# Optimization experiments

Hardware: AMD Instinct MI355X
Metric: run time of the kernel (lower is better)

## Reference

```python
import jax, jax.numpy as jnp
import numpy as np

K = 1024   # number of NNLS components (theta_1 is K x K)
B = 8192   # batched frames / columns


def setup_inputs() -> dict:
    key = jax.random.key(0)
    k1, k2, k3, k4 = jax.random.split(key, 4)
    # theta_1 = I - AtA / ||AtA||_F  -> near-identity contraction; emulate with
    # identity minus a small random symmetric-ish perturbation.
    pert = jax.random.normal(k1, (K, K), dtype=jnp.float32) * (1.0 / K)
    th1 = jnp.eye(K, dtype=jnp.float32) - pert
    Y = jax.random.uniform(k2, (K, B), dtype=jnp.float32)
    X_old = jax.random.uniform(k3, (K, B), dtype=jnp.float32)
    weight = jax.random.normal(k4, (K, B), dtype=jnp.float32) * 0.1  # theta_2 = Atb/n_AtA
    k = 2  # PGD iteration counter
    return {"th1": th1, "Y": Y, "X_old": X_old, "k": k, "weight": weight}


def reference(th1, Y, X_old, k, weight):
    # One projected-gradient-descent step of NNLS with Nesterov momentum:
    #   new_X = relu(th1 @ Y + weight)
    #   Y_new = new_X + (k-1)/(k+2) * (new_X - X_old)
    kf = jnp.float32(k)
    new_X = jax.nn.relu(jnp.matmul(th1, Y) + weight)          # [K, B]
    momentum = (kf - 1.0) / (kf + 2.0)
    Y_new = new_X + momentum * (new_X - X_old)                # [K, B]
    return (Y_new, new_X, k + 1, weight)
```

## Files before the change

### kernel.cpp

```cpp
#include <hip/hip_runtime.h>
#include <cstdint>


#define KDIM 1024
#define NDIM 8192
#define KB_ELEMS (1024UL * 8192UL)
#define LDA 40

typedef short short8 __attribute__((ext_vector_type(8)));
typedef float f32x4 __attribute__((ext_vector_type(4)));

struct __attribute__((aligned(4))) f4u { float x, y, z, w; };

__device__ __forceinline__ uint32_t pk2(float a, float b) {
  uint32_t ua = __builtin_bit_cast(uint32_t, a) + 0x8000u;
  uint32_t ub = __builtin_bit_cast(uint32_t, b) + 0x8000u;
  return (ua >> 16) | (ub & 0xFFFF0000u);
}

__global__ __launch_bounds__(512, 4) void nnls_gemm(
    const float* __restrict__ th1, const float* __restrict__ Y,
    const float* __restrict__ xold, const int* __restrict__ kin,
    const float* __restrict__ weight, float* __restrict__ out)
{
  __shared__ __align__(16) char smem[32768];
  unsigned short* As = (unsigned short*)smem;
  unsigned short* Bs = (unsigned short*)(smem + 10240);

  const int tid  = threadIdx.x;
  const int lane = tid & 63;
  const int w    = tid >> 6;
  const int wm = w >> 1, wn = w & 1;
  const int quad = lane >> 4, nl = lane & 15;

  const int m0 = blockIdx.y * 128;
  const int n0 = blockIdx.x * 128;

  const int ar = tid >> 3;
  const int ac = tid & 7;
  const float* abase = th1 + (size_t)(m0 + ar) * KDIM + ac * 4;

  const int bn = tid & 127;
  const int bk = (tid >> 7) * 8;
  const float* ybase = Y + (size_t)bk * NDIM + n0 + bn;

  float4 ab[2];
  float  yb[8];
  ab[0] = *(const float4*)(abase);
  ab[1] = *(const float4*)(abase + (size_t)64 * KDIM);
#pragma unroll
  for (int r = 0; r < 8; ++r) yb[r] = ybase[(size_t)r * NDIM];

  f32x4 acc[2][4] = {};

  for (int kt = 0; kt < 32; ++kt) {
    {
      uint2 d0; d0.x = pk2(ab[0].x, ab[0].y); d0.y = pk2(ab[0].z, ab[0].w);
      *(uint2*)&As[ar * LDA + ac * 4] = d0;
      uint2 d1; d1.x = pk2(ab[1].x, ab[1].y); d1.y = pk2(ab[1].z, ab[1].w);
      *(uint2*)&As[(ar + 64) * LDA + ac * 4] = d1;
      uint4 e;
      e.x = pk2(yb[0], yb[1]); e.y = pk2(yb[2], yb[3]);
      e.z = pk2(yb[4], yb[5]); e.w = pk2(yb[6], yb[7]);
      *(uint4*)&Bs[bn * LDA + bk] = e;
    }
    __syncthreads();

    if (kt < 31) {
      const float* an = abase + (kt + 1) * 32;
      ab[0] = *(const float4*)(an);
      ab[1] = *(const float4*)(an + (size_t)64 * KDIM);
      const float* yn = ybase + (size_t)((kt + 1) * 32) * NDIM;
#pragma unroll
      for (int r = 0; r < 8; ++r) yb[r] = yn[(size_t)r * NDIM];
    }

    short8 af[2], bf[4];
#pragma unroll
    for (int i = 0; i < 2; ++i)
      af[i] = *(const short8*)&As[(wm * 32 + i * 16 + nl) * LDA + quad * 8];
#pragma unroll
    for (int j = 0; j < 4; ++j)
      bf[j] = *(const short8*)&Bs[(wn * 64 + j * 16 + nl) * LDA + quad * 8];
#pragma unroll
    for (int i = 0; i < 2; ++i)
#pragma unroll
      for (int j = 0; j < 4; ++j)
        acc[i][j] = __builtin_amdgcn_mfma_f32_16x16x32_bf16(af[i], bf[j], acc[i][j], 0, 0, 0);

    __syncthreads();
  }

  const float kf  = (float)kin[0];
  const float mom = (kf - 1.0f) / (kf + 2.0f);
  float* ep = (float*)smem + w * 1024;
  const int lr = lane >> 2;
  const int cb = (lane & 3) * 16;
  const int swzR = 16 * ((lr >> 2) & 1) + 4 * (lr & 3);

#pragma unroll
  for (int i = 0; i < 2; ++i) {
#pragma unroll
    for (int j = 0; j < 4; ++j)
#pragma unroll
      for (int r = 0; r < 4; ++r) {
        const int wrow = quad * 4 + r;
        const int colp = (j * 16 + nl) ^ (16 * (quad & 1) + 4 * r);
        ep[wrow * 64 + colp] = acc[i][j][r];
      }
    __syncthreads();

    const int mg = m0 + wm * 32 + i * 16 + lr;
#pragma unroll
    for (int t = 0; t < 4; ++t) {
      const int colp = (cb + 4 * t) ^ swzR;
      const float4 cv = *(const float4*)&ep[lr * 64 + colp];
      const int ng = n0 + wn * 64 + cb + 4 * t;
      const size_t idx = (size_t)mg * NDIM + ng;
      const float4 wv = *(const float4*)&weight[idx];
      const float4 xo = *(const float4*)&xold[idx];
      float4 nx, yn;
      nx.x = fmaxf(cv.x + wv.x, 0.0f); nx.y = fmaxf(cv.y + wv.y, 0.0f);
      nx.z = fmaxf(cv.z + wv.z, 0.0f); nx.w = fmaxf(cv.w + wv.w, 0.0f);
      yn.x = nx.x + mom * (nx.x - xo.x); yn.y = nx.y + mom * (nx.y - xo.y);
      yn.z = nx.z + mom * (nx.z - xo.z); yn.w = nx.w + mom * (nx.w - xo.w);
      *(float4*)&out[idx] = yn;
      *(float4*)&out[KB_ELEMS + idx] = nx;
      f4u s; s.x = wv.x; s.y = wv.y; s.z = wv.z; s.w = wv.w;
      *(f4u*)&out[2 * KB_ELEMS + 1 + idx] = s;
    }
    __syncthreads();
  }

  if (blockIdx.x == 0 && blockIdx.y == 0 && tid == 0)
    out[2 * KB_ELEMS] = (float)(kin[0] + 1);
}

extern "C" void kernel_launch(void* const* d_in, const int* in_sizes, int n_in,
                              void* d_out, int out_size, void* d_ws, size_t ws_size,
                              hipStream_t stream) {
  const float* th1  = (const float*)d_in[0];
  const float* Y    = (const float*)d_in[1];
  const float* xold = (const float*)d_in[2];
  const int*   kin  = (const int*)d_in[3];
  const float* wgt  = (const float*)d_in[4];
  float* out = (float*)d_out;

  dim3 grid(NDIM / 128, KDIM / 128);
  nnls_gemm<<<grid, 512, 0, stream>>>(th1, Y, xold, kin, wgt, out);
}
```

Baseline: 251.7 us.

## Double-buffer LDS tiles and restructure epilogue to drop per-stage barriers

```diff
diff --git a/kernel.cpp b/kernel.cpp
--- a/kernel.cpp
+++ b/kernel.cpp
@@ -23,9 +23,11 @@
     const float* __restrict__ xold, const int* __restrict__ kin,
     const float* __restrict__ weight, float* __restrict__ out)
 {
-  __shared__ __align__(16) char smem[32768];
-  unsigned short* As = (unsigned short*)smem;
-  unsigned short* Bs = (unsigned short*)(smem + 10240);
+  __shared__ __align__(16) char smem[40960];
+  unsigned short* As0 = (unsigned short*)smem;
+  unsigned short* Bs0 = (unsigned short*)(smem + 10240);
+  unsigned short* As1 = (unsigned short*)(smem + 20480);
+  unsigned short* Bs1 = (unsigned short*)(smem + 30720);
 
   const int tid  = threadIdx.x;
   const int lane = tid & 63;
@@ -53,16 +55,20 @@
 
   f32x4 acc[2][4] = {};
 
+#pragma unroll 2
   for (int kt = 0; kt < 32; ++kt) {
+    unsigned short* Asp = (kt & 1) ? As1 : As0;
+    unsigned short* Bsp = (kt & 1) ? Bs1 : Bs0;
+
     {
       uint2 d0; d0.x = pk2(ab[0].x, ab[0].y); d0.y = pk2(ab[0].z, ab[0].w);
-      *(uint2*)&As[ar * LDA + ac * 4] = d0;
+      *(uint2*)&Asp[ar * LDA + ac * 4] = d0;
       uint2 d1; d1.x = pk2(ab[1].x, ab[1].y); d1.y = pk2(ab[1].z, ab[1].w);
-      *(uint2*)&As[(ar + 64) * LDA + ac * 4] = d1;
+      *(uint2*)&Asp[(ar + 64) * LDA + ac * 4] = d1;
       uint4 e;
       e.x = pk2(yb[0], yb[1]); e.y = pk2(yb[2], yb[3]);
       e.z = pk2(yb[4], yb[5]); e.w = pk2(yb[6], yb[7]);
-      *(uint4*)&Bs[bn * LDA + bk] = e;
+      *(uint4*)&Bsp[bn * LDA + bk] = e;
     }
     __syncthreads();
 
@@ -78,45 +84,39 @@
     short8 af[2], bf[4];
 #pragma unroll
     for (int i = 0; i < 2; ++i)
-      af[i] = *(const short8*)&As[(wm * 32 + i * 16 + nl) * LDA + quad * 8];
+      af[i] = *(const short8*)&Asp[(wm * 32 + i * 16 + nl) * LDA + quad * 8];
 #pragma unroll
     for (int j = 0; j < 4; ++j)
-      bf[j] = *(const short8*)&Bs[(wn * 64 + j * 16 + nl) * LDA + quad * 8];
+      bf[j] = *(const short8*)&Bsp[(wn * 64 + j * 16 + nl) * LDA + quad * 8];
 #pragma unroll
     for (int i = 0; i < 2; ++i)
 #pragma unroll
       for (int j = 0; j < 4; ++j)
         acc[i][j] = __builtin_amdgcn_mfma_f32_16x16x32_bf16(af[i], bf[j], acc[i][j], 0, 0, 0);
-
-    __syncthreads();
   }
+  __syncthreads();
 
   const float kf  = (float)kin[0];
   const float mom = (kf - 1.0f) / (kf + 2.0f);
-  float* ep = (float*)smem + w * 1024;
-  const int lr = lane >> 2;
-  const int cb = (lane & 3) * 16;
-  const int swzR = 16 * ((lr >> 2) & 1) + 4 * (lr & 3);
+  float* ep = (float*)smem + w * 1088;
+  const int u  = lane >> 4;
+  const int mc = lane & 15;
 
 #pragma unroll
   for (int i = 0; i < 2; ++i) {
 #pragma unroll
     for (int j = 0; j < 4; ++j)
 #pragma unroll
-      for (int r = 0; r < 4; ++r) {
-        const int wrow = quad * 4 + r;
-        const int colp = (j * 16 + nl) ^ (16 * (quad & 1) + 4 * r);
-        ep[wrow * 64 + colp] = acc[i][j][r];
-      }
-    __syncthreads();
+      for (int r = 0; r < 4; ++r)
+        ep[(quad * 4 + r) * 68 + (j * 16 + nl)] = acc[i][j][r];
 
-    const int mg = m0 + wm * 32 + i * 16 + lr;
+    const int mgb = m0 + wm * 32 + i * 16;
 #pragma unroll
     for (int t = 0; t < 4; ++t) {
-      const int colp = (cb + 4 * t) ^ swzR;
-      const float4 cv = *(const float4*)&ep[lr * 64 + colp];
-      const int ng = n0 + wn * 64 + cb + 4 * t;
-      const size_t idx = (size_t)mg * NDIM + ng;
+      const int row = t * 4 + u;
+      const float4 cv = *(const float4*)&ep[row * 68 + mc * 4];
+      const int ng = n0 + wn * 64 + mc * 4;
+      const size_t idx = (size_t)(mgb + row) * NDIM + ng;
       const float4 wv = *(const float4*)&weight[idx];
       const float4 xo = *(const float4*)&xold[idx];
       float4 nx, yn;
@@ -129,7 +129,6 @@
       f4u s; s.x = wv.x; s.y = wv.y; s.z = wv.z; s.w = wv.w;
       *(f4u*)&out[2 * KB_ELEMS + 1 + idx] = s;
     }
-    __syncthreads();
   }
 
   if (blockIdx.x == 0 && blockIdx.y == 0 && tid == 0)
```

New measurement: 221.0 us. 12.2% less time.
